# Performance work log

Measured on AMD Instinct MI355X. Metric: run time of the kernel, lower is better.

## Reference

```python
import jax, jax.numpy as jnp
import numpy as np

N_SIGNALS = 2048
HID = 16  # importance_hidden_dim


def _layernorm(x, g, b, eps=1e-5):
    mu = jnp.mean(x, axis=-1, keepdims=True)
    var = jnp.mean((x - mu) ** 2, axis=-1, keepdims=True)
    return (x - mu) / jnp.sqrt(var + eps) * g + b


def _gelu(x):
    return jax.nn.gelu(x, approximate=False)  # torch nn.GELU default (erf)


def _pairwise_features(p):
    # p: [n, 15] normalized params
    dt = jnp.abs(p[:, None, 5] - p[None, :, 5])
    dra = jnp.abs(p[:, None, 3] - p[None, :, 3])
    ddec = jnp.abs(p[:, None, 4] - p[None, :, 4])
    sky_sep = jnp.sqrt(dra ** 2 + ddec ** 2)
    m1 = p[:, 0] * 95 + 5
    m2 = p[:, 1] * 95 + 5
    mc = (m1 * m2) ** 0.6 / (m1 + m2) ** 0.2  # chirp mass
    mass_sim = 1.0 / (1.0 + jnp.abs(mc[:, None] - mc[None, :]) / 30.0)
    f_isco = 220.0 / (m1 + m2)
    freq_overlap = jnp.exp(-jnp.abs(f_isco[:, None] - f_isco[None, :]) / 100.0)
    dist = p[:, 2] * 2950 + 50
    dist_ratio = jnp.minimum(dist[:, None], dist[None, :]) / jnp.maximum(dist[:, None], dist[None, :])
    dpsi = jnp.abs(p[:, None, 7] - p[None, :, 7])
    # [n, n, 8]
    return jnp.stack([dt, sky_sep, mass_sim, freq_overlap, dist_ratio, dpsi, dra, ddec], axis=-1)


def setup_inputs() -> dict:
    key = jax.random.key(0)
    ks = jax.random.split(key, 16)
    n = N_SIGNALS
    params_batch = jax.random.uniform(ks[0], (n, 15), dtype=jnp.float32)
    def lin(k, out_d, in_d):
        lim = 1.0 / np.sqrt(in_d)
        kw, kb = jax.random.split(k)
        w = jax.random.uniform(kw, (out_d, in_d), minval=-lim, maxval=lim, dtype=jnp.float32)
        b = jax.random.uniform(kb, (out_d,), minval=-lim, maxval=lim, dtype=jnp.float32)
        return w, b
    iw1, ib1 = lin(ks[1], HID, 8)
    iw2, ib2 = lin(ks[2], 1, HID)
    ow1, ob1 = lin(ks[3], 32, 8)
    ow2, ob2 = lin(ks[4], 16, 32)
    return {
        "params_batch": params_batch,
        "iw1": iw1, "ib1": ib1,
        "ig1": jnp.ones((HID,), jnp.float32), "ibt1": jnp.zeros((HID,), jnp.float32),
        "iw2": iw2, "ib2": ib2,
        "ow1": ow1, "ob1": ob1,
        "og1": jnp.ones((32,), jnp.float32), "obt1": jnp.zeros((32,), jnp.float32),
        "ow2": ow2, "ob2": ob2,
    }


def reference(params_batch, iw1, ib1, ig1, ibt1, iw2, ib2, ow1, ob1, og1, obt1, ow2, ob2):
    n = params_batch.shape[0]
    feats = _pairwise_features(params_batch)  # [n, n, 8]
    # importance net (dropout is identity at inference)
    h = _gelu(_layernorm(jnp.einsum('ijf,hf->ijh', feats, iw1) + ib1, ig1, ibt1))
    logits = jnp.einsum('ijh,oh->ijo', h, iw2)[..., 0] + ib2[0]  # [n, n]
    # exclude self-pairs (j == i) from the softmax, matching the i != j loop
    diag = jnp.eye(n, dtype=bool)
    logits = jnp.where(diag, -jnp.inf, logits)
    attn = jax.nn.softmax(logits, axis=1)  # [n, n]
    weighted = jnp.einsum('ij,ijf->if', attn, feats)  # [n, 8]
    # overlap net
    h2 = _gelu(_layernorm(weighted @ ow1.T + ob1, og1, obt1))
    return h2 @ ow2.T + ob2  # [n, 16]
```

## Files before the change

### kernel.cpp

```cpp
#include <hip/hip_runtime.h>

#define N_SIG 2048
#define NT    32
#define N_OFFDIAG_BLOCKS 992
#define N_PAIR_BLOCKS 1024

__device__ __forceinline__ float frcp(float x) { return __builtin_amdgcn_rcpf(x); }

__device__ __forceinline__ float erf_div_sqrt2(float y) {
    const float ay = fabsf(y);
    const float t  = frcp(fmaf(0.23164454f, ay, 1.f));
    const float p  = t * fmaf(t, fmaf(t, fmaf(t, fmaf(t, 1.061405429f, -1.453152027f),
                                              1.421413741f), -0.284496736f), 0.254829592f);
    const float e  = __expf(-0.5f * ay * ay);
    return copysignf(fmaf(-p, e, 1.f), y);
}

__global__ void derive_k(const float* __restrict__ p, float* __restrict__ dv,
                         float* __restrict__ acc) {
    int j = blockIdx.x * blockDim.x + threadIdx.x;
    if (j >= N_SIG) return;
    #pragma unroll
    for (int k = 0; k < 9; k++) acc[j * 9 + k] = 0.f;
    const float* pj = p + j * 15;
    float m1 = pj[0] * 95.f + 5.f, m2 = pj[1] * 95.f + 5.f;
    float mc = powf(m1 * m2, 0.6f) / powf(m1 + m2, 0.2f);
    float fisco = 220.f / (m1 + m2);
    float dist = pj[2] * 2950.f + 50.f;
    float4* o = (float4*)(dv + j * 8);
    o[0] = make_float4(pj[5], pj[3], pj[4], mc);
    o[1] = make_float4(fisco, dist, pj[7], 0.f);
}

__global__ __launch_bounds__(256) void pair_k(
    const float* __restrict__ dv,
    const float* __restrict__ iw1, const float* __restrict__ ib1,
    const float* __restrict__ ig1, const float* __restrict__ ibt1,
    const float* __restrict__ iw2,
    float* __restrict__ acc)
{
    __shared__ float4 sColA[64], sColB[64];
    __shared__ __align__(16) float sW1[128];
    __shared__ __align__(16) float sEC[64];
    __shared__ float part[9 * 256];

    const int b = blockIdx.x;
    int ti, tj, half;
    bool diag;
    if (b < N_OFFDIAG_BLOCKS) {
        const int tileId = b >> 1;
        half = b & 1;
        int k = tileId, row = 0;
        while (k >= NT - 1 - row) { k -= NT - 1 - row; row++; }
        ti = row; tj = row + 1 + k;
        diag = false;
    } else {
        ti = tj = b - N_OFFDIAG_BLOCKS;
        half = 0;
        diag = true;
    }
    const int rbase = ti * 64, cbase = tj * 64;

    const int tid = threadIdx.x;
    const float4* dv4 = (const float4*)dv;

    if (tid < 64)  { sColA[tid] = dv4[(cbase + tid) * 2]; sColB[tid] = dv4[(cbase + tid) * 2 + 1]; }
    if (tid >= 64 && tid < 192) sW1[tid - 64] = iw1[tid - 64];
    if (tid >= 192 && tid < 208) {
        int h = tid - 192;
        sEC[h * 4 + 0] = ib1[h]; sEC[h * 4 + 1] = ig1[h];
        sEC[h * 4 + 2] = ibt1[h]; sEC[h * 4 + 3] = 0.5f * iw2[h];
    }
    __syncthreads();

    const int w = tid >> 6, l = tid & 63;
    const int gi = rbase + l;
    const float4 r0 = dv4[gi * 2], r1 = dv4[gi * 2 + 1];
    const float ti_ = r0.x, rai = r0.y, deci = r0.z, mci = r0.w;
    const float fi = r1.x, disti = r1.y, psii = r1.z;

    const int sstep = diag ? 4 : 8;
    const int sbase = diag ? (w + 1) : (half * 4 + w);

    float rowacc[9], colacc[9];
    #pragma unroll
    for (int q = 0; q < 9; q++) { rowacc[q] = 0.f; colacc[q] = 0.f; }

    const float4* sW4  = (const float4*)sW1;
    const float4* sEC4 = (const float4*)sEC;

    for (int t = 0; t < 8; t++) {
        const int s  = sbase + sstep * t;
        const int dj = (l + s) & 63;
        const float4 c0 = sColA[dj], c1 = sColB[dj];

        const float dra  = fabsf(rai - c0.y), ddec = fabsf(deci - c0.z);
        float f[8];
        f[0] = fabsf(ti_ - c0.x);
        f[1] = __builtin_amdgcn_sqrtf(fmaf(dra, dra, ddec * ddec));
        f[2] = frcp(fmaf(fabsf(mci - c0.w), 0.033333333f, 1.f));
        f[3] = __expf(fabsf(fi - c1.x) * -0.01f);
        f[4] = fminf(disti, c1.y) * frcp(fmaxf(disti, c1.y));
        f[5] = fabsf(psii - c1.z);
        f[6] = dra; f[7] = ddec;

        float z[16];
        float s1 = 0.f, s2 = 0.f;
        #pragma unroll
        for (int h = 0; h < 16; h++) {
            const float4 w0 = sW4[h * 2];
            const float4 w1 = sW4[h * 2 + 1];
            float zv = sEC4[h].x;
            zv = fmaf(w0.x, f[0], zv); zv = fmaf(w0.y, f[1], zv);
            zv = fmaf(w0.z, f[2], zv); zv = fmaf(w0.w, f[3], zv);
            zv = fmaf(w1.x, f[4], zv); zv = fmaf(w1.y, f[5], zv);
            zv = fmaf(w1.z, f[6], zv); zv = fmaf(w1.w, f[7], zv);
            z[h] = zv;
            s1 += zv; s2 = fmaf(zv, zv, s2);
        }
        const float mu  = s1 * 0.0625f;
        const float var = fmaf(-mu, mu, s2 * 0.0625f);
        const float inv = __builtin_amdgcn_rsqf(var + 1e-5f);

        float logit = 0.f;
        #pragma unroll
        for (int h = 0; h < 16; h++) {
            const float4 c = sEC4[h];
            const float y = fmaf((z[h] - mu) * inv, c.y, c.z);
            logit = fmaf(y * c.w, 1.f + erf_div_sqrt2(y), logit);
        }
        float e = __expf(logit);
        if (diag && s == 32 && l >= 32) e = 0.f;

        rowacc[8] += e; colacc[8] += e;
        #pragma unroll
        for (int q = 0; q < 8; q++) {
            rowacc[q] = fmaf(e, f[q], rowacc[q]);
            colacc[q] = fmaf(e, f[q], colacc[q]);
        }
        if (t + 1 < 8) {
            const int src = (l + sstep) & 63;
            #pragma unroll
            for (int q = 0; q < 9; q++) colacc[q] = __shfl(colacc[q], src);
        }
    }

    const int stag = b & 63;

    #pragma unroll
    for (int q = 0; q < 9; q++) part[q * 256 + w * 64 + l] = rowacc[q];
    __syncthreads();
    if (tid < 192) {
        const int sig = (tid + stag) & 63;
        #pragma unroll
        for (int r = 0; r < 3; r++) {
            const int q = (tid >> 6) * 3 + r;
            const float* pp = part + q * 256 + sig;
            unsafeAtomicAdd(&acc[(rbase + sig) * 9 + q], pp[0] + pp[64] + pp[128] + pp[192]);
        }
    }
    __syncthreads();

    const int s_last = sbase + sstep * 7;
    const int cfin = (l + s_last) & 63;
    #pragma unroll
    for (int q = 0; q < 9; q++) part[q * 256 + w * 64 + cfin] = colacc[q];
    __syncthreads();
    if (tid < 192) {
        const int sig = (tid + stag) & 63;
        #pragma unroll
        for (int r = 0; r < 3; r++) {
            const int q = (tid >> 6) * 3 + r;
            const float* pp = part + q * 256 + sig;
            unsafeAtomicAdd(&acc[(cbase + sig) * 9 + q], pp[0] + pp[64] + pp[128] + pp[192]);
        }
    }
}

__global__ void out_k(const float* __restrict__ acc,
                      const float* __restrict__ ow1, const float* __restrict__ ob1,
                      const float* __restrict__ og1, const float* __restrict__ obt1,
                      const float* __restrict__ ow2, const float* __restrict__ ob2,
                      float* __restrict__ out)
{
    __shared__ float h2s[32];
    const int i = blockIdx.x, t = threadIdx.x;
    if (t < 32) {
        const float invL = frcp(acc[i * 9 + 8]);
        float z2 = ob1[t];
        #pragma unroll
        for (int f = 0; f < 8; f++) z2 = fmaf(ow1[t * 8 + f], acc[i * 9 + f] * invL, z2);
        float mu = z2;
        #pragma unroll
        for (int off = 16; off > 0; off >>= 1) mu += __shfl_xor(mu, off);
        mu *= (1.f / 32.f);
        const float d = z2 - mu;
        float var = d * d;
        #pragma unroll
        for (int off = 16; off > 0; off >>= 1) var += __shfl_xor(var, off);
        var *= (1.f / 32.f);
        const float y = d * __builtin_amdgcn_rsqf(var + 1e-5f) * og1[t] + obt1[t];
        h2s[t] = 0.5f * y * (1.f + erf_div_sqrt2(y));
    }
    __syncthreads();
    if (t < 16) {
        float o = ob2[t];
        #pragma unroll
        for (int k = 0; k < 32; k++) o = fmaf(ow2[t * 32 + k], h2s[k], o);
        out[i * 16 + t] = o;
    }
}

extern "C" void kernel_launch(void* const* d_in, const int* in_sizes, int n_in,
                              void* d_out, int out_size, void* d_ws, size_t ws_size,
                              hipStream_t stream) {
    const float* p    = (const float*)d_in[0];
    const float* iw1  = (const float*)d_in[1];
    const float* ib1  = (const float*)d_in[2];
    const float* ig1  = (const float*)d_in[3];
    const float* ibt1 = (const float*)d_in[4];
    const float* iw2  = (const float*)d_in[5];
    const float* ow1  = (const float*)d_in[7];
    const float* ob1  = (const float*)d_in[8];
    const float* og1  = (const float*)d_in[9];
    const float* obt1 = (const float*)d_in[10];
    const float* ow2  = (const float*)d_in[11];
    const float* ob2  = (const float*)d_in[12];

    float* dv  = (float*)d_ws;
    float* acc = (float*)d_ws + N_SIG * 8;

    derive_k<<<N_SIG / 256, 256, 0, stream>>>(p, dv, acc);
    pair_k<<<N_PAIR_BLOCKS, 256, 0, stream>>>(dv, iw1, ib1, ig1, ibt1, iw2, acc);
    out_k<<<N_SIG, 64, 0, stream>>>(acc, ow1, ob1, og1, obt1, ow2, ob2,
                                    (float*)d_out);
}
```

Before: 139.8 us.

## Replace atomic accumulation with per-block partial buffers reduced in output kernel

```diff
diff --git a/kernel.cpp b/kernel.cpp
--- a/kernel.cpp
+++ b/kernel.cpp
@@ -4,6 +4,8 @@
 #define NT    32
 #define N_OFFDIAG_BLOCKS 992
 #define N_PAIR_BLOCKS 1024
+#define DV_FLOATS   (N_SIG * 8)
+#define PART_FLOATS (32 * 64 * 9 * 64)
 
 __device__ __forceinline__ float frcp(float x) { return __builtin_amdgcn_rcpf(x); }
 
@@ -16,12 +18,15 @@
     return copysignf(fmaf(-p, e, 1.f), y);
 }
 
+template<bool ZERO_ACC>
 __global__ void derive_k(const float* __restrict__ p, float* __restrict__ dv,
                          float* __restrict__ acc) {
     int j = blockIdx.x * blockDim.x + threadIdx.x;
     if (j >= N_SIG) return;
-    #pragma unroll
-    for (int k = 0; k < 9; k++) acc[j * 9 + k] = 0.f;
+    if constexpr (ZERO_ACC) {
+        #pragma unroll
+        for (int k = 0; k < 9; k++) acc[j * 9 + k] = 0.f;
+    }
     const float* pj = p + j * 15;
     float m1 = pj[0] * 95.f + 5.f, m2 = pj[1] * 95.f + 5.f;
     float mc = powf(m1 * m2, 0.6f) / powf(m1 + m2, 0.2f);
@@ -32,6 +37,7 @@
     o[1] = make_float4(fisco, dist, pj[7], 0.f);
 }
 
+template<bool USE_PART>
 __global__ __launch_bounds__(256) void pair_k(
     const float* __restrict__ dv,
     const float* __restrict__ iw1, const float* __restrict__ ib1,
@@ -42,7 +48,8 @@
     __shared__ float4 sColA[64], sColB[64];
     __shared__ __align__(16) float sW1[128];
     __shared__ __align__(16) float sEC[64];
-    __shared__ float part[9 * 256];
+    __shared__ float partR[9 * 256];
+    __shared__ float partC[USE_PART ? 9 * 256 : 1];
 
     const int b = blockIdx.x;
     int ti, tj, half;
@@ -145,51 +152,92 @@
         }
     }
 
-    const int stag = b & 63;
-
-    #pragma unroll
-    for (int q = 0; q < 9; q++) part[q * 256 + w * 64 + l] = rowacc[q];
-    __syncthreads();
-    if (tid < 192) {
-        const int sig = (tid + stag) & 63;
-        #pragma unroll
-        for (int r = 0; r < 3; r++) {
-            const int q = (tid >> 6) * 3 + r;
-            const float* pp = part + q * 256 + sig;
-            unsafeAtomicAdd(&acc[(rbase + sig) * 9 + q], pp[0] + pp[64] + pp[128] + pp[192]);
-        }
-    }
-    __syncthreads();
-
     const int s_last = sbase + sstep * 7;
     const int cfin = (l + s_last) & 63;
-    #pragma unroll
-    for (int q = 0; q < 9; q++) part[q * 256 + w * 64 + cfin] = colacc[q];
-    __syncthreads();
-    if (tid < 192) {
-        const int sig = (tid + stag) & 63;
-        #pragma unroll
-        for (int r = 0; r < 3; r++) {
-            const int q = (tid >> 6) * 3 + r;
-            const float* pp = part + q * 256 + sig;
-            unsafeAtomicAdd(&acc[(cbase + sig) * 9 + q], pp[0] + pp[64] + pp[128] + pp[192]);
-        }
-    }
-}
-
-__global__ void out_k(const float* __restrict__ acc,
+
+    if constexpr (USE_PART) {
+        #pragma unroll
+        for (int q = 0; q < 9; q++) partR[q * 256 + w * 64 + l]    = rowacc[q];
+        #pragma unroll
+        for (int q = 0; q < 9; q++) partC[q * 256 + w * 64 + cfin] = colacc[q];
+        __syncthreads();
+        if (tid < 192) {
+            const int sig = tid & 63;
+            float* __restrict__ pr = acc + ((ti * 64 + (2 * tj + half)) * 9) * 64;
+            float* __restrict__ pc = acc + ((tj * 64 + (2 * ti + 1 - half)) * 9) * 64;
+            #pragma unroll
+            for (int r = 0; r < 3; r++) {
+                const int q = (tid >> 6) * 3 + r;
+                const float* ppR = partR + q * 256 + sig;
+                pr[q * 64 + sig] = ppR[0] + ppR[64] + ppR[128] + ppR[192];
+                const float* ppC = partC + q * 256 + sig;
+                pc[q * 64 + sig] = ppC[0] + ppC[64] + ppC[128] + ppC[192];
+            }
+        }
+    } else {
+        const int stag = b & 63;
+        #pragma unroll
+        for (int q = 0; q < 9; q++) partR[q * 256 + w * 64 + l] = rowacc[q];
+        __syncthreads();
+        if (tid < 192) {
+            const int sig = (tid + stag) & 63;
+            #pragma unroll
+            for (int r = 0; r < 3; r++) {
+                const int q = (tid >> 6) * 3 + r;
+                const float* pp = partR + q * 256 + sig;
+                unsafeAtomicAdd(&acc[(rbase + sig) * 9 + q], pp[0] + pp[64] + pp[128] + pp[192]);
+            }
+        }
+        __syncthreads();
+        #pragma unroll
+        for (int q = 0; q < 9; q++) partR[q * 256 + w * 64 + cfin] = colacc[q];
+        __syncthreads();
+        if (tid < 192) {
+            const int sig = (tid + stag) & 63;
+            #pragma unroll
+            for (int r = 0; r < 3; r++) {
+                const int q = (tid >> 6) * 3 + r;
+                const float* pp = partR + q * 256 + sig;
+                unsafeAtomicAdd(&acc[(cbase + sig) * 9 + q], pp[0] + pp[64] + pp[128] + pp[192]);
+            }
+        }
+    }
+}
+
+template<bool USE_PART>
+__global__ void out_k(const float* __restrict__ accp,
                       const float* __restrict__ ow1, const float* __restrict__ ob1,
                       const float* __restrict__ og1, const float* __restrict__ obt1,
                       const float* __restrict__ ow2, const float* __restrict__ ob2,
                       float* __restrict__ out)
 {
     __shared__ float h2s[32];
-    const int i = blockIdx.x, t = threadIdx.x;
+    const int t = threadIdx.x;
+    int i;
+    float a9[9];
+    if constexpr (USE_PART) {
+        const int b = blockIdx.x;
+        i = (b & 7) * 256 + (b >> 3);
+        const int g = i >> 6, sig = i & 63;
+        #pragma unroll
+        for (int q = 0; q < 9; q++) {
+            float v = accp[(((g * 64 + t) * 9) + q) * 64 + sig];
+            #pragma unroll
+            for (int off = 32; off > 0; off >>= 1) v += __shfl_xor(v, off);
+            a9[q] = v;
+        }
+    } else {
+        i = blockIdx.x;
+        if (t < 32) {
+            #pragma unroll
+            for (int q = 0; q < 9; q++) a9[q] = accp[i * 9 + q];
+        }
+    }
     if (t < 32) {
-        const float invL = frcp(acc[i * 9 + 8]);
+        const float invL = frcp(a9[8]);
         float z2 = ob1[t];
         #pragma unroll
-        for (int f = 0; f < 8; f++) z2 = fmaf(ow1[t * 8 + f], acc[i * 9 + f] * invL, z2);
+        for (int f = 0; f < 8; f++) z2 = fmaf(ow1[t * 8 + f], a9[f] * invL, z2);
         float mu = z2;
         #pragma unroll
         for (int off = 16; off > 0; off >>= 1) mu += __shfl_xor(mu, off);
@@ -227,11 +275,20 @@
     const float* ow2  = (const float*)d_in[11];
     const float* ob2  = (const float*)d_in[12];
 
-    float* dv  = (float*)d_ws;
-    float* acc = (float*)d_ws + N_SIG * 8;
-
-    derive_k<<<N_SIG / 256, 256, 0, stream>>>(p, dv, acc);
-    pair_k<<<N_PAIR_BLOCKS, 256, 0, stream>>>(dv, iw1, ib1, ig1, ibt1, iw2, acc);
-    out_k<<<N_SIG, 64, 0, stream>>>(acc, ow1, ob1, og1, obt1, ow2, ob2,
-                                    (float*)d_out);
-}
+    float* dv = (float*)d_ws;
+    const bool use_part = ws_size >= (size_t)(DV_FLOATS + PART_FLOATS) * sizeof(float);
+
+    if (use_part) {
+        float* part = dv + DV_FLOATS;
+        derive_k<false><<<N_SIG / 256, 256, 0, stream>>>(p, dv, nullptr);
+        pair_k<true><<<N_PAIR_BLOCKS, 256, 0, stream>>>(dv, iw1, ib1, ig1, ibt1, iw2, part);
+        out_k<true><<<N_SIG, 64, 0, stream>>>(part, ow1, ob1, og1, obt1, ow2, ob2,
+                                              (float*)d_out);
+    } else {
+        float* acc = dv + DV_FLOATS;
+        derive_k<true><<<N_SIG / 256, 256, 0, stream>>>(p, dv, acc);
+        pair_k<false><<<N_PAIR_BLOCKS, 256, 0, stream>>>(dv, iw1, ib1, ig1, ibt1, iw2, acc);
+        out_k<false><<<N_SIG, 64, 0, stream>>>(acc, ow1, ob1, og1, obt1, ow2, ob2,
+                                               (float*)d_out);
+    }
+}
```

After: 118.6 us (median of 2 runs). 15.2% less time.
